# Kernel tuning notes

Hardware: AMD Instinct MI355X
Metric: run time of the kernel (lower is better)

## Reference

```python
import jax, jax.numpy as jnp
import numpy as np

N = 100000       # num nodes
E = 1600000      # num edges
D_IN = 32
D_HID = 32
D_OUT = 32
K = 3            # Chebyshev order (number of terms)


def setup_inputs() -> dict:
    key = jax.random.key(0)
    k1, k2, k3, k4, k5, k6 = jax.random.split(key, 6)
    x = jax.random.normal(k1, (N, D_IN), dtype=jnp.float32)
    edge_index = jax.random.randint(k2, (2, E), 0, N, dtype=jnp.int64)
    s1 = 1.0 / np.sqrt(D_IN)
    s2 = 1.0 / np.sqrt(D_HID)
    W1 = jax.random.uniform(k3, (K, D_IN, D_HID), jnp.float32, -s1, s1)
    b1 = jax.random.uniform(k4, (D_HID,), jnp.float32, -s1, s1)
    W2 = jax.random.uniform(k5, (K, D_HID, D_OUT), jnp.float32, -s2, s2)
    b2 = jax.random.uniform(k6, (D_OUT,), jnp.float32, -s2, s2)
    return {"x": x, "edge_index": edge_index, "W1": W1, "b1": b1, "W2": W2, "b2": b2}


def _prop(x, row, col, w):
    # L_hat @ x : gather along col, scale by edge weight, scatter-add to row.
    # (diagonal of the rescaled Laplacian cancels to 0 in PyG ChebConv with
    #  sym normalization and lambda_max=2, so only off-diagonal edges remain)
    return jax.ops.segment_sum(w[:, None] * x[col], row, num_segments=N)


def _cheb_conv(x, row, col, w, W, b):
    # Chebyshev recurrence: Tx0 = x, Tx1 = L_hat x, Tx_k = 2 L_hat Tx_{k-1} - Tx_{k-2}
    k_terms = W.shape[0]
    Tx0 = x
    out = Tx0 @ W[0]
    if k_terms > 1:
        Tx1 = _prop(Tx0, row, col, w)
        out = out + Tx1 @ W[1]
        for k in range(2, k_terms):
            Tx2 = 2.0 * _prop(Tx1, row, col, w) - Tx0
            out = out + Tx2 @ W[k]
            Tx0, Tx1 = Tx1, Tx2
    return out + b


def reference(x, edge_index, W1, b1, W2, b2):
    row, col = edge_index[0], edge_index[1]
    mask = (row != col).astype(x.dtype)            # remove_self_loops
    deg = jax.ops.segment_sum(mask, row, num_segments=N)
    dinv = jnp.where(deg > 0, 1.0 / jnp.sqrt(jnp.maximum(deg, 1.0)), 0.0)
    w = -mask * dinv[row] * dinv[col]              # scaled Laplacian off-diagonal weights
    x0 = x
    h = jax.nn.relu(_cheb_conv(x, row, col, w, W1, b1))
    h = _cheb_conv(h, row, col, w, W2, b2)
    return h + x0
```

## Files before the change

kernel.cpp:

```cpp
#include <hip/hip_runtime.h>

#define NN 100000
#define EE 1600000
#define DD 32
#define NBUK 391
#define BROWS 256
#define TILE 4096
#define NT 391

#define TOTP   106176
#define ENT2SZ 2084352
#define ZTOT   ((TOTP * 16 + ENT2SZ * 4) / 16)
#define ZPB    ((ZTOT + NT - 1) / NT)

__constant__ int c_cap[9]   = {0, 2944, 56320, 43520, 2944, 256, 64, 64, 64};
__constant__ int c_pbase[9] = {0, 0, 2944, 59264, 102784, 105728, 105984, 106048, 106112};
__constant__ int c_ebase[9] = {0, 0, 23552, 924672, 1969152, 2063360, 2073600, 2076672, 2080256};

typedef unsigned int uint;
typedef unsigned short ushort;
typedef unsigned char uchar;
typedef __attribute__((ext_vector_type(8))) short bf16x8;
typedef __attribute__((ext_vector_type(4))) float f32x4;
typedef __attribute__((ext_vector_type(2))) float f32x2;

typedef __attribute__((ext_vector_type(4))) uint u32x4v;
typedef __attribute__((ext_vector_type(2))) uint u32x2v;
typedef __attribute__((ext_vector_type(4))) int i32x4v;
typedef __attribute__((ext_vector_type(4))) float f32x4v;

__device__ __forceinline__ uint4 ntld(const uint4* p) {
    u32x4v v = __builtin_nontemporal_load((const u32x4v*)p);
    uint4 r; r.x = v.x; r.y = v.y; r.z = v.z; r.w = v.w; return r;
}
__device__ __forceinline__ uint2 ntld(const uint2* p) {
    u32x2v v = __builtin_nontemporal_load((const u32x2v*)p);
    uint2 r; r.x = v.x; r.y = v.y; return r;
}
__device__ __forceinline__ int4 ntld(const int4* p) {
    i32x4v v = __builtin_nontemporal_load((const i32x4v*)p);
    int4 r; r.x = v.x; r.y = v.y; r.z = v.z; r.w = v.w; return r;
}
__device__ __forceinline__ float4 ntld(const float4* p) {
    f32x4v v = __builtin_nontemporal_load((const f32x4v*)p);
    float4 r; r.x = v.x; r.y = v.y; r.z = v.z; r.w = v.w; return r;
}
__device__ __forceinline__ int   ntld(const int* p)   { return __builtin_nontemporal_load(p); }
__device__ __forceinline__ float ntld(const float* p) { return __builtin_nontemporal_load(p); }
__device__ __forceinline__ void ntst(uint4* p, uint4 v) {
    u32x4v w; w.x = v.x; w.y = v.y; w.z = v.z; w.w = v.w;
    __builtin_nontemporal_store(w, (u32x4v*)p);
}
__device__ __forceinline__ void ntst(int4* p, int4 v) {
    uint4 u; u.x = (uint)v.x; u.y = (uint)v.y; u.z = (uint)v.z; u.w = (uint)v.w;
    ntst((uint4*)p, u);
}
__device__ __forceinline__ void ntst(uint2* p, uint2 v) {
    u32x2v w; w.x = v.x; w.y = v.y;
    __builtin_nontemporal_store(w, (u32x2v*)p);
}
__device__ __forceinline__ void ntst(int* p, int v)     { __builtin_nontemporal_store(v, p); }
__device__ __forceinline__ void ntst(float* p, float v) { __builtin_nontemporal_store(v, p); }

__device__ __forceinline__ ushort f2b(float f) {
    uint u = __float_as_uint(f);
    u += 0x7fffu + ((u >> 16) & 1u);
    return (ushort)(u >> 16);
}
__device__ __forceinline__ uint f2e4(float f) {
    uint u = __float_as_uint(f);
    uint s = (u >> 24) & 0x80u;
    float a = fabsf(f) * 0x1p-120f;
    uint g = __float_as_uint(a);
    g += 0x7FFFFu + ((g >> 20) & 1u);
    uint m = g >> 20;
    if (m > 0x7Eu) m = 0x7Eu;
    return s | m;
}
__device__ __forceinline__ bf16x8 as_bf16x8(uint4 v) {
    union { uint4 u; bf16x8 b; } cv; cv.u = v; return cv.b;
}
__device__ __forceinline__ void acc8(float* acc, uint2 v) {
#pragma unroll
    for (int wi = 0; wi < 2; ++wi) {
        uint w = (&v.x)[wi];
        f32x2 lo = __builtin_amdgcn_cvt_pk_f32_fp8((int)w, false);
        f32x2 hi = __builtin_amdgcn_cvt_pk_f32_fp8((int)w, true);
        acc[wi * 4 + 0] += lo.x;
        acc[wi * 4 + 1] += lo.y;
        acc[wi * 4 + 2] += hi.x;
        acc[wi * 4 + 3] += hi.y;
    }
}


__global__ void k_part(const int* __restrict__ ei, int* __restrict__ pairs2,
                       ushort* __restrict__ ofs, uint4* __restrict__ zbase,
                       int* __restrict__ ctail) {
    {
        int z0 = blockIdx.x * ZPB;
        int ze = z0 + ZPB; if (ze > ZTOT) ze = ZTOT;
        uint4 zz; zz.x = 0; zz.y = 0; zz.z = 0; zz.w = 0;
        for (int i = z0 + threadIdx.x; i < ze; i += 256) ntst(zbase + i, zz);
    }
    if (blockIdx.x == 0 && threadIdx.x < 16) ctail[threadIdx.x] = 0;
    __shared__ int hist[512];
    __shared__ int h2[256];
    __shared__ int pref[512];
    __shared__ int spk[TILE];
    int t = threadIdx.x;
    hist[t] = 0; hist[t + 256] = 0;
    __syncthreads();
    int e0 = blockIdx.x * TILE;
    int pk[16], rk[16], bb[16];
#pragma unroll
    for (int k = 0; k < 16; ++k) {
        int e = e0 + t + k * 256;
        bb[k] = -1;
        if (e < EE) {
            int r = ntld(ei + e), c = ntld(ei + EE + e);
            if (r != c) {
                bb[k] = r >> 8;
                pk[k] = (r & (BROWS - 1)) | (c << 8);
                rk[k] = atomicAdd(&hist[bb[k]], 1);
            }
        }
    }
    __syncthreads();
    int a = hist[2 * t], b = hist[2 * t + 1];
    h2[t] = a + b;
    __syncthreads();
    for (int d = 1; d < 256; d <<= 1) {
        int v = h2[t];
        int u = (t >= d) ? h2[t - d] : 0;
        __syncthreads();
        h2[t] = v + u;
        __syncthreads();
    }
    int base = t ? h2[t - 1] : 0;
    pref[2 * t] = base;
    pref[2 * t + 1] = base + a;
    __syncthreads();
#pragma unroll
    for (int k = 0; k < 16; ++k)
        if (bb[k] >= 0) spk[pref[bb[k]] + rk[k]] = pk[k];
    for (int q = t; q <= NBUK; q += 256)
        ofs[q * NT + blockIdx.x] = (ushort)pref[q];
    __syncthreads();
    int tot = pref[NBUK];
    int* dst = pairs2 + blockIdx.x * TILE;
    for (int i = t; i < tot; i += 256) ntst(dst + i, spk[i]);
}


__global__ void k_build2(const int* __restrict__ pairs2, const ushort* __restrict__ ofs,
                         int* __restrict__ ctail,
                         int* __restrict__ ent2, int4* __restrict__ pdesc,
                         const float* __restrict__ x, uint2* __restrict__ xb,
                         uint* __restrict__ xb8,
                         const float* __restrict__ W1, const float* __restrict__ W2,
                         ushort* __restrict__ wb1, ushort* __restrict__ wb2,
                         uint* __restrict__ t1b8, uint* __restrict__ hb8) {
    if (blockIdx.x == NBUK) {
        for (int i = threadIdx.x; i < 6144; i += 256) {
            const float* W = W1; ushort* wb = wb1;
            int ii = i;
            if (ii >= 3072) { ii -= 3072; W = W2; wb = wb2; }
            int term = ii >> 10, rem = ii & 1023;
            int h = rem >> 9, lane = (rem >> 3) & 63, j = rem & 7;
            int k = ((lane >> 4) << 3) + j;
            int col = (h << 4) | (lane & 15);
            float val = W[term * 1024 + k * 32 + col];
            if (term == 0) val -= W[2 * 1024 + k * 32 + col];
            wb[ii] = f2b(val);
        }
        if (threadIdx.x >= 64 && threadIdx.x < 72) xb8[NN * 8 + threadIdx.x - 64] = 0;
        if (threadIdx.x >= 72 && threadIdx.x < 80) t1b8[NN * 8 + threadIdx.x - 72] = 0;
        if (threadIdx.x >= 80 && threadIdx.x < 88) hb8[NN * 8 + threadIdx.x - 80] = 0;
        return;
    }
    __shared__ int lcnt[BROWS];
    __shared__ int lh[16];
    __shared__ int gb[16];
    __shared__ int sofs[BROWS];
    __shared__ float sdinv[BROWS];
    __shared__ uchar scls[BROWS];
    __shared__ ushort so0[NT];
    __shared__ int h2s[256];
    __shared__ int segb[512];
    __shared__ int slab[BROWS * 64];
    int b = blockIdx.x, t = threadIdx.x;
    lcnt[t] = 0;
    if (t < 16) lh[t] = 0;
    int l0 = 0, l1 = 0;
    {
        int i0 = 2 * t, i1 = 2 * t + 1;
        if (i0 < NT) {
            int s0 = ofs[b * NT + i0];
            so0[i0] = (ushort)s0;
            l0 = (int)ofs[(b + 1) * NT + i0] - s0;
        }
        if (i1 < NT) {
            int s1 = ofs[b * NT + i1];
            so0[i1] = (ushort)s1;
            l1 = (int)ofs[(b + 1) * NT + i1] - s1;
        }
    }
    h2s[t] = l0 + l1;
    for (int i = t; i < BROWS * 64; i += 256) slab[i] = NN;
    __syncthreads();
    for (int d = 1; d < 256; d <<= 1) {
        int v = h2s[t];
        int u = (t >= d) ? h2s[t - d] : 0;
        __syncthreads();
        h2s[t] = v + u;
        __syncthreads();
    }
    int sb = t ? h2s[t - 1] : 0;
    segb[2 * t] = sb;
    segb[2 * t + 1] = sb + l0;
    __syncthreads();
    int T = h2s[255];
    for (int i = t; i < T; i += 256) {
        int lo = 0, hi = NT - 1;
#pragma unroll
        for (int s = 0; s < 9; ++s) {
            int mid = (lo + hi + 1) >> 1;
            bool c = segb[mid] <= i;
            lo = c ? mid : lo;
            hi = c ? hi : mid - 1;
        }
        int v = ntld(pairs2 + lo * TILE + (int)so0[lo] + (i - segb[lo]));
        int lr = v & (BROWS - 1);
        int pos = atomicAdd(&lcnt[lr], 1);
        if (pos < 64) slab[(lr << 6) + pos] = (int)((uint)v >> 8);
    }
    __syncthreads();
    int n = b * BROWS + t;
    int cpl = 0, lrank = 0;
    float dv = 0.0f;
    if (n < NN) {
        int d = lcnt[t];
        int ms = d > 64 ? 64 : d;
        int cls = (ms + 7) >> 3;
        cpl = cls ? cls : 1;
        dv = d > 0 ? rsqrtf((float)d) : 0.0f;
        lrank = atomicAdd(&lh[cpl], 1);
    }
    sdinv[t] = dv;
    __syncthreads();
    if (t < 16) gb[t] = lh[t] ? atomicAdd(&ctail[t], lh[t]) : 0;
    __syncthreads();
    int myofs = -1;
    if (n < NN) {
        int rank = gb[cpl] + lrank;
        if (rank < c_cap[cpl]) {
            myofs = c_ebase[cpl] + rank * (cpl << 3);
            int4 pv; pv.x = n; pv.y = cpl; pv.z = (int)__float_as_uint(dv); pv.w = 0;
            pdesc[c_pbase[cpl] + rank] = pv;
        }
    }
    sofs[t] = myofs;
    scls[t] = (uchar)cpl;
    __syncthreads();
    for (int i = t; i < BROWS * 16; i += 256) {
        int row = i >> 4, piece = i & 15;
        int ofs2 = sofs[row];
        if (ofs2 >= 0 && piece < (scls[row] << 1)) {
            int4 v = *(const int4*)&slab[(row << 6) + (piece << 2)];
            ntst((int4*)&ent2[ofs2 + (piece << 2)], v);
        }
    }
    int base4 = b * 2048;
    for (int i = t; i < 2048; i += 256) {
        int row = i >> 3;
        if (b * BROWS + row < NN) {
            float4 v = ntld((const float4*)x + base4 + i);
            uint2 b2;
            b2.x = (uint)f2b(v.x) | ((uint)f2b(v.y) << 16);
            b2.y = (uint)f2b(v.z) | ((uint)f2b(v.w) << 16);
            ntst(xb + base4 + i, b2);
            float dvr = sdinv[row];
            xb8[base4 + i] = f2e4(dvr * v.x) | (f2e4(dvr * v.y) << 8)
                           | (f2e4(dvr * v.z) << 16) | (f2e4(dvr * v.w) << 24);
        }
    }
}


__global__ void k_prop(const int4* __restrict__ pdesc, const int* __restrict__ ent2,
                       const uint2* __restrict__ src8d,
                       uint2* __restrict__ dst8d,
                       uint4* __restrict__ dstbq) {
    int tid = blockIdx.x * blockDim.x + threadIdx.x;
    int g = tid >> 3;
    int sub = tid & 3, h = (tid >> 2) & 1;
    int4 pd = ntld(pdesc + g);
    constexpr int kPB[9] = {0, 0, 2944, 59264, 102784, 105728, 105984, 106048, 106112};
    constexpr int kEB[9] = {0, 0, 23552, 924672, 1969152, 2063360, 2073600, 2076672, 2080256};
    int cls = 1, pb = 0, eb = 0;
#pragma unroll
    for (int c = 2; c <= 8; ++c)
        if (g >= kPB[c]) { cls = c; pb = kPB[c]; eb = kEB[c]; }
    const int* ep = ent2 + eb + (g - pb) * (cls << 3);
    int mr = cls << 3;
    float acc[8] = {0, 0, 0, 0, 0, 0, 0, 0};
    for (int i = h * 8; i < mr; i += 16) {
        uint4 C0 = ntld((const uint4*)(ep + i));
        uint4 C1 = ntld((const uint4*)(ep + i + 4));
        uint2 v0 = src8d[(C0.x << 2) + sub];
        uint2 v1 = src8d[(C0.y << 2) + sub];
        uint2 v2 = src8d[(C0.z << 2) + sub];
        uint2 v3 = src8d[(C0.w << 2) + sub];
        uint2 v4 = src8d[(C1.x << 2) + sub];
        uint2 v5 = src8d[(C1.y << 2) + sub];
        uint2 v6 = src8d[(C1.z << 2) + sub];
        uint2 v7 = src8d[(C1.w << 2) + sub];
        acc8(acc, v0); acc8(acc, v1); acc8(acc, v2); acc8(acc, v3);
        acc8(acc, v4); acc8(acc, v5); acc8(acc, v6); acc8(acc, v7);
    }
    if (pd.y == 0) return;
    int n = pd.x;
    float dn = __uint_as_float((uint)pd.z);
    float s = -dn;
#pragma unroll
    for (int k = 0; k < 8; ++k)
        acc[k] = s * (acc[k] + __shfl_xor(acc[k], 4, 64));
    if (h == 0) {
        uint4 ob;
#pragma unroll
        for (int wi = 0; wi < 4; ++wi)
            (&ob.x)[wi] = (uint)f2b(acc[wi * 2]) | ((uint)f2b(acc[wi * 2 + 1]) << 16);
        ntst(dstbq + (n << 2) + sub, ob);
    } else {
        uint2 o8;
        o8.x = f2e4(dn * acc[0]) | (f2e4(dn * acc[1]) << 8)
             | (f2e4(dn * acc[2]) << 16) | (f2e4(dn * acc[3]) << 24);
        o8.y = f2e4(dn * acc[4]) | (f2e4(dn * acc[5]) << 8)
             | (f2e4(dn * acc[6]) << 16) | (f2e4(dn * acc[7]) << 24);
        ntst(dst8d + (n << 2) + sub, o8);
    }
}


__global__ void __launch_bounds__(256) k_prop2c(
        const int4* __restrict__ pdesc, const int* __restrict__ ent2,
        const uint2* __restrict__ src8d,
        const uint4* __restrict__ t0g,
        const uint4* __restrict__ t1g,
        const ushort* __restrict__ wb, const float* __restrict__ bias,
        const float* __restrict__ residf, float* __restrict__ outf,
        ushort* __restrict__ outb, uchar* __restrict__ outb8, int do_relu) {
    __shared__ ushort sT[32 * 40];
    __shared__ int   sn[32];
    __shared__ float sdv[32];
    int tid = blockIdx.x * 256 + threadIdx.x;
    int g = tid >> 3, sub = tid & 3, h = (tid >> 2) & 1;
    int slot = threadIdx.x >> 3;
    int4 pd = ntld(pdesc + g);
    constexpr int kPB[9] = {0, 0, 2944, 59264, 102784, 105728, 105984, 106048, 106112};
    constexpr int kEB[9] = {0, 0, 23552, 924672, 1969152, 2063360, 2073600, 2076672, 2080256};
    int cls = 1, pb = 0, eb = 0;
#pragma unroll
    for (int c = 2; c <= 8; ++c)
        if (g >= kPB[c]) { cls = c; pb = kPB[c]; eb = kEB[c]; }
    const int* ep = ent2 + eb + (g - pb) * (cls << 3);
    int mr = cls << 3;
    float acc[8] = {0, 0, 0, 0, 0, 0, 0, 0};
    for (int i = h * 8; i < mr; i += 16) {
        uint4 C0 = ntld((const uint4*)(ep + i));
        uint4 C1 = ntld((const uint4*)(ep + i + 4));
        uint2 v0 = src8d[(C0.x << 2) + sub];
        uint2 v1 = src8d[(C0.y << 2) + sub];
        uint2 v2 = src8d[(C0.z << 2) + sub];
        uint2 v3 = src8d[(C0.w << 2) + sub];
        uint2 v4 = src8d[(C1.x << 2) + sub];
        uint2 v5 = src8d[(C1.y << 2) + sub];
        uint2 v6 = src8d[(C1.z << 2) + sub];
        uint2 v7 = src8d[(C1.w << 2) + sub];
        acc8(acc, v0); acc8(acc, v1); acc8(acc, v2); acc8(acc, v3);
        acc8(acc, v4); acc8(acc, v5); acc8(acc, v6); acc8(acc, v7);
    }
    if (pd.y != 0) {
        float dn = __uint_as_float((uint)pd.z);
        float s = -2.0f * dn;
#pragma unroll
        for (int k = 0; k < 8; ++k)
            acc[k] = s * (acc[k] + __shfl_xor(acc[k], 4, 64));
        if (h == 0) {
            uint4 ow;
#pragma unroll
            for (int wi = 0; wi < 4; ++wi)
                (&ow.x)[wi] = (uint)f2b(acc[wi * 2]) | ((uint)f2b(acc[wi * 2 + 1]) << 16);
            *(uint4*)&sT[slot * 40 + sub * 8] = ow;
            if (sub == 0) { sn[slot] = pd.x; sdv[slot] = dn; }
        }
    } else if ((threadIdx.x & 7) == 0) {
        sn[slot] = -1;
    }
    __syncthreads();
    if (threadIdx.x >= 128) return;
    int wv = threadIdx.x >> 6, lane = threadIdx.x & 63;
    int q = lane >> 4, lr = lane & 15;
    const uint4* wq = (const uint4*)wb;
    bf16x8 bf[3][2];
#pragma unroll
    for (int t = 0; t < 3; ++t)
#pragma unroll
        for (int hh = 0; hh < 2; ++hh)
            bf[t][hh] = as_bf16x8(wq[((t * 2 + hh) << 6) + lane]);
    float bias0 = bias[lr], bias1 = bias[16 + lr];
    uint4 z; z.x = 0; z.y = 0; z.z = 0; z.w = 0;
    int lrow = wv * 16 + lr;
    int an = sn[lrow];
    bool ok = an >= 0;
    int ai = (an << 2) + q;
    bf16x8 a0 = as_bf16x8(ok ? ntld(t0g + ai) : z);
    bf16x8 a1 = as_bf16x8(ok ? ntld(t1g + ai) : z);
    bf16x8 a2 = *(const bf16x8*)&sT[lrow * 40 + q * 8];
    f32x4 c0 = {0.f, 0.f, 0.f, 0.f};
    f32x4 c1 = {0.f, 0.f, 0.f, 0.f};
    c0 = __builtin_amdgcn_mfma_f32_16x16x32_bf16(a0, bf[0][0], c0, 0, 0, 0);
    c0 = __builtin_amdgcn_mfma_f32_16x16x32_bf16(a1, bf[1][0], c0, 0, 0, 0);
    c0 = __builtin_amdgcn_mfma_f32_16x16x32_bf16(a2, bf[2][0], c0, 0, 0, 0);
    c1 = __builtin_amdgcn_mfma_f32_16x16x32_bf16(a0, bf[0][1], c1, 0, 0, 0);
    c1 = __builtin_amdgcn_mfma_f32_16x16x32_bf16(a1, bf[1][1], c1, 0, 0, 0);
    c1 = __builtin_amdgcn_mfma_f32_16x16x32_bf16(a2, bf[2][1], c1, 0, 0, 0);
#pragma unroll
    for (int r = 0; r < 4; ++r) {
        int ls = wv * 16 + (q << 2) + r;
        int nd = sn[ls];
        if (nd < 0) continue;
        float v0 = c0[r] + bias0;
        float v1 = c1[r] + bias1;
        if (do_relu) { v0 = fmaxf(v0, 0.0f); v1 = fmaxf(v1, 0.0f); }
        if (outb) {
            float dvv = sdv[ls];
            outb[nd * DD + lr] = f2b(v0);
            outb[nd * DD + 16 + lr] = f2b(v1);
            outb8[nd * DD + lr] = (uchar)f2e4(dvv * v0);
            outb8[nd * DD + 16 + lr] = (uchar)f2e4(dvv * v1);
        } else {
            ntst(outf + nd * DD + lr, v0 + ntld(residf + nd * DD + lr));
            ntst(outf + nd * DD + 16 + lr, v1 + ntld(residf + nd * DD + 16 + lr));
        }
    }
}


extern "C" void kernel_launch(void* const* d_in, const int* in_sizes, int n_in,
                              void* d_out, int out_size, void* d_ws, size_t ws_size,
                              hipStream_t stream) {
    const float* x  = (const float*)d_in[0];
    const int*   ei = (const int*)d_in[1];
    const float* W1 = (const float*)d_in[2];
    const float* b1 = (const float*)d_in[3];
    const float* W2 = (const float*)d_in[4];
    const float* b2 = (const float*)d_in[5];
    float* out = (float*)d_out;

    char* wsp = (char*)d_ws;
    size_t off = 0;
    auto take = [&](size_t bytes) {
        char* p = wsp + off;
        off = (off + bytes + 255) & ~(size_t)255;
        return p;
    };
    int*    ctail  = (int*)take((size_t)16 * 4);
    int4*   pdesc  = (int4*)take((size_t)TOTP * 16);
    int*    ent2   = (int*)take((size_t)ENT2SZ * 4);
    ushort* ofs    = (ushort*)take((size_t)(NBUK + 1) * NT * 2);
    int*    pairs2 = (int*)take((size_t)NT * TILE * 4);
    ushort* wb1    = (ushort*)take((size_t)3072 * 2);
    ushort* wb2    = (ushort*)take((size_t)3072 * 2);
    ushort* xb     = (ushort*)take((size_t)NN * DD * 2);
    ushort* t1b    = (ushort*)take((size_t)NN * DD * 2);
    ushort* hb     = (ushort*)take((size_t)NN * DD * 2);
    uchar*  xb8    = (uchar*)take((size_t)(NN + 1) * DD);
    uchar*  t1b8   = (uchar*)take((size_t)(NN + 1) * DD);
    uchar*  hb8    = (uchar*)take((size_t)(NN + 1) * DD);


    k_part  <<<NT, 256, 0, stream>>>(ei, pairs2, ofs, (uint4*)pdesc, ctail);
    k_build2<<<NBUK + 1, 256, 0, stream>>>(pairs2, ofs, ctail, ent2, pdesc,
                                           x, (uint2*)xb, (uint*)xb8,
                                           W1, W2, wb1, wb2,
                                           (uint*)t1b8, (uint*)hb8);

    const int pgrid = TOTP * 8 / 256;
    k_prop  <<<pgrid, 256, 0, stream>>>(pdesc, ent2, (const uint2*)xb8,
                                        (uint2*)t1b8, (uint4*)t1b);
    k_prop2c<<<pgrid, 256, 0, stream>>>(pdesc, ent2, (const uint2*)t1b8,
                                        (const uint4*)xb, (const uint4*)t1b,
                                        wb1, b1, nullptr, nullptr,
                                        hb, hb8, 1);
    k_prop  <<<pgrid, 256, 0, stream>>>(pdesc, ent2, (const uint2*)hb8,
                                        (uint2*)t1b8, (uint4*)t1b);
    k_prop2c<<<pgrid, 256, 0, stream>>>(pdesc, ent2, (const uint2*)t1b8,
                                        (const uint4*)hb, (const uint4*)t1b,
                                        wb2, b2, x, out,
                                        nullptr, nullptr, 0);
}
```

Baseline: 212.7 us.

## Use 4 threads per node with 16-byte fp8 gathers in propagation kernels

Each destination node is now handled by 4 threads instead of 8, and each thread gathers 16 bytes (16 fp8 features) per neighbor rather than 8. This halves the thread count and gather instruction count per edge and lets each k_prop2c block cover 64 nodes with all 256 threads doing the MMA epilogue. The cost is more registers per thread (16 accumulators) and half the grid, so there is less latency hiding per gathered byte.

```diff
diff --git a/kernel.cpp b/kernel.cpp
--- a/kernel.cpp
+++ b/kernel.cpp
@@ -80,9 +80,9 @@
 __device__ __forceinline__ bf16x8 as_bf16x8(uint4 v) {
     union { uint4 u; bf16x8 b; } cv; cv.u = v; return cv.b;
 }
-__device__ __forceinline__ void acc8(float* acc, uint2 v) {
-#pragma unroll
-    for (int wi = 0; wi < 2; ++wi) {
+__device__ __forceinline__ void acc16(float* acc, uint4 v) {
+#pragma unroll
+    for (int wi = 0; wi < 4; ++wi) {
         uint w = (&v.x)[wi];
         f32x2 lo = __builtin_amdgcn_cvt_pk_f32_fp8((int)w, false);
         f32x2 hi = __builtin_amdgcn_cvt_pk_f32_fp8((int)w, true);
@@ -289,12 +289,12 @@
 
 
 __global__ void k_prop(const int4* __restrict__ pdesc, const int* __restrict__ ent2,
-                       const uint2* __restrict__ src8d,
-                       uint2* __restrict__ dst8d,
+                       const uint4* __restrict__ src8q,
+                       uint4* __restrict__ dst8q,
                        uint4* __restrict__ dstbq) {
     int tid = blockIdx.x * blockDim.x + threadIdx.x;
-    int g = tid >> 3;
-    int sub = tid & 3, h = (tid >> 2) & 1;
+    int g = tid >> 2;
+    int s2 = tid & 1, h = (tid >> 1) & 1;
     int4 pd = ntld(pdesc + g);
     constexpr int kPB[9] = {0, 0, 2944, 59264, 102784, 105728, 105984, 106048, 106112};
     constexpr int kEB[9] = {0, 0, 23552, 924672, 1969152, 2063360, 2073600, 2076672, 2080256};
@@ -304,59 +304,64 @@
         if (g >= kPB[c]) { cls = c; pb = kPB[c]; eb = kEB[c]; }
     const int* ep = ent2 + eb + (g - pb) * (cls << 3);
     int mr = cls << 3;
-    float acc[8] = {0, 0, 0, 0, 0, 0, 0, 0};
+    float acc[16];
+#pragma unroll
+    for (int k = 0; k < 16; ++k) acc[k] = 0.0f;
     for (int i = h * 8; i < mr; i += 16) {
         uint4 C0 = ntld((const uint4*)(ep + i));
         uint4 C1 = ntld((const uint4*)(ep + i + 4));
-        uint2 v0 = src8d[(C0.x << 2) + sub];
-        uint2 v1 = src8d[(C0.y << 2) + sub];
-        uint2 v2 = src8d[(C0.z << 2) + sub];
-        uint2 v3 = src8d[(C0.w << 2) + sub];
-        uint2 v4 = src8d[(C1.x << 2) + sub];
-        uint2 v5 = src8d[(C1.y << 2) + sub];
-        uint2 v6 = src8d[(C1.z << 2) + sub];
-        uint2 v7 = src8d[(C1.w << 2) + sub];
-        acc8(acc, v0); acc8(acc, v1); acc8(acc, v2); acc8(acc, v3);
-        acc8(acc, v4); acc8(acc, v5); acc8(acc, v6); acc8(acc, v7);
+        uint4 v0 = src8q[(C0.x << 1) + s2];
+        uint4 v1 = src8q[(C0.y << 1) + s2];
+        uint4 v2 = src8q[(C0.z << 1) + s2];
+        uint4 v3 = src8q[(C0.w << 1) + s2];
+        uint4 v4 = src8q[(C1.x << 1) + s2];
+        uint4 v5 = src8q[(C1.y << 1) + s2];
+        uint4 v6 = src8q[(C1.z << 1) + s2];
+        uint4 v7 = src8q[(C1.w << 1) + s2];
+        acc16(acc, v0); acc16(acc, v1); acc16(acc, v2); acc16(acc, v3);
+        acc16(acc, v4); acc16(acc, v5); acc16(acc, v6); acc16(acc, v7);
     }
     if (pd.y == 0) return;
     int n = pd.x;
     float dn = __uint_as_float((uint)pd.z);
     float s = -dn;
 #pragma unroll
-    for (int k = 0; k < 8; ++k)
-        acc[k] = s * (acc[k] + __shfl_xor(acc[k], 4, 64));
+    for (int k = 0; k < 16; ++k)
+        acc[k] = s * (acc[k] + __shfl_xor(acc[k], 2, 64));
     if (h == 0) {
-        uint4 ob;
+        uint4 o0, o1;
+#pragma unroll
+        for (int wi = 0; wi < 4; ++wi) {
+            (&o0.x)[wi] = (uint)f2b(acc[wi * 2]) | ((uint)f2b(acc[wi * 2 + 1]) << 16);
+            (&o1.x)[wi] = (uint)f2b(acc[8 + wi * 2]) | ((uint)f2b(acc[8 + wi * 2 + 1]) << 16);
+        }
+        ntst(dstbq + (n << 2) + (s2 << 1), o0);
+        ntst(dstbq + (n << 2) + (s2 << 1) + 1, o1);
+    } else {
+        uint4 o8;
 #pragma unroll
         for (int wi = 0; wi < 4; ++wi)
-            (&ob.x)[wi] = (uint)f2b(acc[wi * 2]) | ((uint)f2b(acc[wi * 2 + 1]) << 16);
-        ntst(dstbq + (n << 2) + sub, ob);
-    } else {
-        uint2 o8;
-        o8.x = f2e4(dn * acc[0]) | (f2e4(dn * acc[1]) << 8)
-             | (f2e4(dn * acc[2]) << 16) | (f2e4(dn * acc[3]) << 24);
-        o8.y = f2e4(dn * acc[4]) | (f2e4(dn * acc[5]) << 8)
-             | (f2e4(dn * acc[6]) << 16) | (f2e4(dn * acc[7]) << 24);
-        ntst(dst8d + (n << 2) + sub, o8);
+            (&o8.x)[wi] = f2e4(dn * acc[wi * 4]) | (f2e4(dn * acc[wi * 4 + 1]) << 8)
+                        | (f2e4(dn * acc[wi * 4 + 2]) << 16) | (f2e4(dn * acc[wi * 4 + 3]) << 24);
+        ntst(dst8q + (n << 1) + s2, o8);
     }
 }
 
 
 __global__ void __launch_bounds__(256) k_prop2c(
         const int4* __restrict__ pdesc, const int* __restrict__ ent2,
-        const uint2* __restrict__ src8d,
+        const uint4* __restrict__ src8q,
         const uint4* __restrict__ t0g,
         const uint4* __restrict__ t1g,
         const ushort* __restrict__ wb, const float* __restrict__ bias,
         const float* __restrict__ residf, float* __restrict__ outf,
         ushort* __restrict__ outb, uchar* __restrict__ outb8, int do_relu) {
-    __shared__ ushort sT[32 * 40];
-    __shared__ int   sn[32];
-    __shared__ float sdv[32];
+    __shared__ ushort sT[64 * 40];
+    __shared__ int   sn[64];
+    __shared__ float sdv[64];
     int tid = blockIdx.x * 256 + threadIdx.x;
-    int g = tid >> 3, sub = tid & 3, h = (tid >> 2) & 1;
-    int slot = threadIdx.x >> 3;
+    int g = tid >> 2, s2 = tid & 1, h = (tid >> 1) & 1;
+    int slot = threadIdx.x >> 2;
     int4 pd = ntld(pdesc + g);
     constexpr int kPB[9] = {0, 0, 2944, 59264, 102784, 105728, 105984, 106048, 106112};
     constexpr int kEB[9] = {0, 0, 23552, 924672, 1969152, 2063360, 2073600, 2076672, 2080256};
@@ -366,40 +371,44 @@
         if (g >= kPB[c]) { cls = c; pb = kPB[c]; eb = kEB[c]; }
     const int* ep = ent2 + eb + (g - pb) * (cls << 3);
     int mr = cls << 3;
-    float acc[8] = {0, 0, 0, 0, 0, 0, 0, 0};
+    float acc[16];
+#pragma unroll
+    for (int k = 0; k < 16; ++k) acc[k] = 0.0f;
     for (int i = h * 8; i < mr; i += 16) {
         uint4 C0 = ntld((const uint4*)(ep + i));
         uint4 C1 = ntld((const uint4*)(ep + i + 4));
-        uint2 v0 = src8d[(C0.x << 2) + sub];
-        uint2 v1 = src8d[(C0.y << 2) + sub];
-        uint2 v2 = src8d[(C0.z << 2) + sub];
-        uint2 v3 = src8d[(C0.w << 2) + sub];
-        uint2 v4 = src8d[(C1.x << 2) + sub];
-        uint2 v5 = src8d[(C1.y << 2) + sub];
-        uint2 v6 = src8d[(C1.z << 2) + sub];
-        uint2 v7 = src8d[(C1.w << 2) + sub];
-        acc8(acc, v0); acc8(acc, v1); acc8(acc, v2); acc8(acc, v3);
-        acc8(acc, v4); acc8(acc, v5); acc8(acc, v6); acc8(acc, v7);
+        uint4 v0 = src8q[(C0.x << 1) + s2];
+        uint4 v1 = src8q[(C0.y << 1) + s2];
+        uint4 v2 = src8q[(C0.z << 1) + s2];
+        uint4 v3 = src8q[(C0.w << 1) + s2];
+        uint4 v4 = src8q[(C1.x << 1) + s2];
+        uint4 v5 = src8q[(C1.y << 1) + s2];
+        uint4 v6 = src8q[(C1.z << 1) + s2];
+        uint4 v7 = src8q[(C1.w << 1) + s2];
+        acc16(acc, v0); acc16(acc, v1); acc16(acc, v2); acc16(acc, v3);
+        acc16(acc, v4); acc16(acc, v5); acc16(acc, v6); acc16(acc, v7);
     }
     if (pd.y != 0) {
         float dn = __uint_as_float((uint)pd.z);
         float s = -2.0f * dn;
 #pragma unroll
-        for (int k = 0; k < 8; ++k)
-            acc[k] = s * (acc[k] + __shfl_xor(acc[k], 4, 64));
+        for (int k = 0; k < 16; ++k)
+            acc[k] = s * (acc[k] + __shfl_xor(acc[k], 2, 64));
         if (h == 0) {
-            uint4 ow;
-#pragma unroll
-            for (int wi = 0; wi < 4; ++wi)
-                (&ow.x)[wi] = (uint)f2b(acc[wi * 2]) | ((uint)f2b(acc[wi * 2 + 1]) << 16);
-            *(uint4*)&sT[slot * 40 + sub * 8] = ow;
-            if (sub == 0) { sn[slot] = pd.x; sdv[slot] = dn; }
-        }
-    } else if ((threadIdx.x & 7) == 0) {
+            uint4 ow0, ow1;
+#pragma unroll
+            for (int wi = 0; wi < 4; ++wi) {
+                (&ow0.x)[wi] = (uint)f2b(acc[wi * 2]) | ((uint)f2b(acc[wi * 2 + 1]) << 16);
+                (&ow1.x)[wi] = (uint)f2b(acc[8 + wi * 2]) | ((uint)f2b(acc[8 + wi * 2 + 1]) << 16);
+            }
+            *(uint4*)&sT[slot * 40 + s2 * 16] = ow0;
+            *(uint4*)&sT[slot * 40 + s2 * 16 + 8] = ow1;
+            if (s2 == 0) { sn[slot] = pd.x; sdv[slot] = dn; }
+        }
+    } else if ((threadIdx.x & 3) == 0) {
         sn[slot] = -1;
     }
     __syncthreads();
-    if (threadIdx.x >= 128) return;
     int wv = threadIdx.x >> 6, lane = threadIdx.x & 63;
     int q = lane >> 4, lr = lane & 15;
     const uint4* wq = (const uint4*)wb;
@@ -487,16 +496,16 @@
                                            W1, W2, wb1, wb2,
                                            (uint*)t1b8, (uint*)hb8);
 
-    const int pgrid = TOTP * 8 / 256;
-    k_prop  <<<pgrid, 256, 0, stream>>>(pdesc, ent2, (const uint2*)xb8,
-                                        (uint2*)t1b8, (uint4*)t1b);
-    k_prop2c<<<pgrid, 256, 0, stream>>>(pdesc, ent2, (const uint2*)t1b8,
+    const int pgrid = TOTP * 4 / 256;
+    k_prop  <<<pgrid, 256, 0, stream>>>(pdesc, ent2, (const uint4*)xb8,
+                                        (uint4*)t1b8, (uint4*)t1b);
+    k_prop2c<<<pgrid, 256, 0, stream>>>(pdesc, ent2, (const uint4*)t1b8,
                                         (const uint4*)xb, (const uint4*)t1b,
                                         wb1, b1, nullptr, nullptr,
                                         hb, hb8, 1);
-    k_prop  <<<pgrid, 256, 0, stream>>>(pdesc, ent2, (const uint2*)hb8,
-                                        (uint2*)t1b8, (uint4*)t1b);
-    k_prop2c<<<pgrid, 256, 0, stream>>>(pdesc, ent2, (const uint2*)t1b8,
+    k_prop  <<<pgrid, 256, 0, stream>>>(pdesc, ent2, (const uint4*)hb8,
+                                        (uint4*)t1b8, (uint4*)t1b);
+    k_prop2c<<<pgrid, 256, 0, stream>>>(pdesc, ent2, (const uint4*)t1b8,
                                         (const uint4*)hb, (const uint4*)t1b,
                                         wb2, b2, x, out,
                                         nullptr, nullptr, 0);
```

Result: no change. 215.2 us (+1.2%).
